# Kernel optimization log

Hardware: AMD Instinct MI355X
Metric: run time of the kernel (lower is better)

The kernel has to match this reference:

```python
import jax, jax.numpy as jnp
import numpy as np

H = 128            # hidden_dim
R = 16             # num_rbf
L = 3              # num_atom_encoder_layers
LAT = 32           # latent_dim
NUM_ATOM_TYPES = 64
CUTOFF = 5.0       # atom_cutoff
N_RES = 2048
DEG = 16           # avg radius-graph degree
_PATTERN = np.array([19, 20, 21, 22, 23, 24, 25, 22])  # ragged atoms/residue, mean 22


def setup_inputs() -> dict:
    key = jax.random.key(0)
    ks = jax.random.split(key, 16)
    apr = np.tile(_PATTERN, N_RES // len(_PATTERN))        # (N,) atoms per residue
    A = int(apr.sum())                                     # 45056 atoms
    E = A * DEG                                            # 720896 edges
    rng = np.random.default_rng(0)

    def gl(k, shape, fan_in):
        return jax.random.normal(k, shape, jnp.float32) * (fan_in ** -0.5)

    return {
        "atom_coords": jax.random.normal(ks[0], (A, 3), jnp.float32) * 10.0,
        "atom_types": jax.random.randint(ks[1], (A,), 0, NUM_ATOM_TYPES),
        "residue_indices": jnp.asarray(np.repeat(np.arange(N_RES), apr)),
        "residue_types": jax.random.randint(ks[2], (N_RES,), 0, 4),
        "atoms_per_residue": jnp.asarray(apr),
        "edge_src": jnp.asarray(rng.integers(0, A, E)),
        "edge_dst": jnp.asarray(rng.integers(0, A, E)),
        # learned parameters
        "atom_embed": gl(ks[3], (NUM_ATOM_TYPES, H), 1.0),
        "residue_embed": gl(ks[4], (4, H), 1.0),
        "We1": gl(ks[5], (L, 2 * H + R, H), 2 * H + R), "be1": jnp.zeros((L, H)),
        "We2": gl(ks[6], (L, H, H), H), "be2": jnp.zeros((L, H)),
        "Wh1": gl(ks[7], (L, 2 * H, H), 2 * H), "bh1": jnp.zeros((L, H)),
        "Wh2": gl(ks[8], (L, H, H), H), "bh2": jnp.zeros((L, H)),
        "Wq": gl(ks[9], (H, H), H), "bq": jnp.zeros((H,)),
        "Wk": gl(ks[10], (H, H), H), "bk": jnp.zeros((H,)),
        "Wv": gl(ks[11], (H, H), H), "bv": jnp.zeros((H,)),
        "Wmu": gl(ks[12], (H, LAT), H), "bmu": jnp.zeros((LAT,)),
        "Wlv": gl(ks[13], (H, LAT), H) * 0.01, "blv": jnp.full((LAT,), -2.0),
    }


def reference(atom_coords, atom_types, residue_indices, residue_types,
              atoms_per_residue, edge_src, edge_dst,
              atom_embed, residue_embed,
              We1, be1, We2, be2, Wh1, bh1, Wh2, bh2,
              Wq, bq, Wk, bk, Wv, bv, Wmu, bmu, Wlv, blv):
    A = atom_coords.shape[0]
    N = residue_types.shape[0]
    coords = atom_coords - atom_coords.mean(0, keepdims=True)  # center_coords

    # Gaussian radial basis expansion of edge distances
    d = jnp.linalg.norm(coords[edge_src] - coords[edge_dst], axis=-1)  # (E,)
    centers = jnp.linspace(0.0, CUTOFF, R)
    gamma = (R / CUTOFF) ** 2
    edge_attr = jnp.exp(-gamma * (d[:, None] - centers) ** 2)          # (E,R)

    # atom features: atom-type embed + residue-type embed scattered to atoms
    res_emb = residue_embed[residue_types]                             # (N,H)
    h = atom_embed[atom_types] + res_emb[residue_indices]              # (A,H)

    # EGNN layers (update_coords=False): message MLP -> sum-agg -> residual node MLP
    for l in range(L):
        m = jnp.concatenate([h[edge_src], h[edge_dst], edge_attr], axis=-1)  # (E,2H+R)
        m = jax.nn.silu(m @ We1[l] + be1[l])
        m = jax.nn.silu(m @ We2[l] + be2[l])                                  # (E,H)
        agg = jax.ops.segment_sum(m, edge_dst, num_segments=A)               # (A,H)
        u = jnp.concatenate([h, agg], axis=-1)                               # (A,2H)
        u = jax.nn.silu(u @ Wh1[l] + bh1[l])
        h = h + (u @ Wh2[l] + bh2[l])

    # segment (per-residue) attention pooling of atoms -> residues
    q = res_emb @ Wq + bq                                              # (N,H)
    k = h @ Wk + bk                                                    # (A,H)
    v = h @ Wv + bv                                                    # (A,H)
    scores = jnp.sum(q[residue_indices] * k, axis=-1) * (H ** -0.5)    # (A,)
    smax = jax.ops.segment_max(scores, residue_indices, num_segments=N)
    ex = jnp.exp(scores - smax[residue_indices])
    denom = jax.ops.segment_sum(ex, residue_indices, num_segments=N)
    w = ex / denom[residue_indices]
    pooled = jax.ops.segment_sum(w[:, None] * v, residue_indices, num_segments=N)  # (N,H)

    mu = pooled @ Wmu + bmu
    logvar = jnp.clip(pooled @ Wlv + blv, -10.0, 2.0)
    return mu, logvar
```

## Files before the change

### kernel.cpp

```cpp
#include <hip/hip_runtime.h>
#include <hip/hip_bf16.h>

#define H 128
#define LATD 32

typedef __attribute__((ext_vector_type(8))) _Float16 half8t;
typedef __attribute__((ext_vector_type(4))) _Float16 half4t;
typedef __attribute__((ext_vector_type(8))) unsigned short u16x8;
typedef __attribute__((ext_vector_type(4))) float f32x4;

#define OFF_RBF 0
#define OFF_W2  12288
#define OFF_PROJ 61440
#define OFF_H1  159744
#define OFF_H2  258048
#define WP_TOTAL 307200

__device__ __forceinline__ float silu_f(float x) {
  return x * __builtin_amdgcn_rcpf(1.0f + __expf(-x));
}
__device__ __forceinline__ unsigned short f16u(float x) {
  _Float16 hh = (_Float16)x;
  return *(unsigned short*)&hh;
}

template<int K>
__device__ __forceinline__ void mm4x4(const float* X0, int ldx,
                                      const float* __restrict__ W, int c0,
                                      float acc[4][4]) {
  #pragma unroll 4
  for (int k = 0; k < K; k += 4) {
    float4 xv[4], w4[4];
    #pragma unroll
    for (int rr = 0; rr < 4; ++rr) xv[rr] = *(const float4*)(X0 + rr * ldx + k);
    #pragma unroll
    for (int kk = 0; kk < 4; ++kk) w4[kk] = *(const float4*)(W + (size_t)(k + kk) * H + c0);
    const float* x = (const float*)xv;
    const float* w = (const float*)w4;
    #pragma unroll
    for (int rr = 0; rr < 4; ++rr)
      #pragma unroll
      for (int cc = 0; cc < 4; ++cc)
        acc[rr][cc] += x[rr*4+0]*w[cc] + x[rr*4+1]*w[4+cc] +
                       x[rr*4+2]*w[8+cc] + x[rr*4+3]*w[12+cc];
  }
}

__global__ void k_init_h(const float* __restrict__ atom_embed,
                         const float* __restrict__ residue_embed,
                         const int* __restrict__ atype,
                         const int* __restrict__ ridx,
                         const int* __restrict__ rtype,
                         float* __restrict__ h, unsigned short* __restrict__ hb, int A) {
  int i = blockIdx.x * blockDim.x + threadIdx.x;
  if (i >= A * H) return;
  int a = i >> 7, j = i & 127;
  float v = atom_embed[atype[a] * H + j] + residue_embed[rtype[ridx[a]] * H + j];
  h[i] = v;
  hb[i] = f16u(v);
}

__global__ void k_dist(const float* __restrict__ coords,
                       const int* __restrict__ esrc, const int* __restrict__ edst,
                       float* __restrict__ dbuf, int E) {
  int e = blockIdx.x * blockDim.x + threadIdx.x;
  if (e >= E) return;
  int s = esrc[e], t = edst[e];
  float dx = coords[3*s+0] - coords[3*t+0];
  float dy = coords[3*s+1] - coords[3*t+1];
  float dz = coords[3*s+2] - coords[3*t+2];
  dbuf[e] = sqrtf(dx*dx + dy*dy + dz*dz);
}

__global__ void k_starts(const int* __restrict__ ridx, int* __restrict__ starts, int A) {
  int a = blockIdx.x * blockDim.x + threadIdx.x;
  if (a >= A) return;
  if (a == 0 || ridx[a] != ridx[a-1]) starts[ridx[a]] = a;
}

__global__ void k_hist(const int* __restrict__ edst, int* __restrict__ cnt, int E) {
  int e = blockIdx.x * blockDim.x + threadIdx.x;
  if (e < E) atomicAdd(&cnt[edst[e]], 1);
}

__global__ __launch_bounds__(1024) void k_scanA(const int* __restrict__ cnt,
                                                int* __restrict__ cursor,
                                                int* __restrict__ bsum, int A) {
  __shared__ int buf[1024];
  int tid = threadIdx.x;
  int i = blockIdx.x * 1024 + tid;
  int v = (i < A) ? cnt[i] : 0;
  buf[tid] = v;
  __syncthreads();
  #pragma unroll
  for (int off = 1; off < 1024; off <<= 1) {
    int nv = (tid >= off) ? buf[tid - off] : 0;
    __syncthreads();
    buf[tid] += nv;
    __syncthreads();
  }
  if (i < A) cursor[i] = buf[tid] - v;
  if (tid == 1023) bsum[blockIdx.x] = buf[1023];
}

__global__ void k_scanB(int* __restrict__ bsum, int nb) {
  int lane = threadIdx.x;
  int v = (lane < nb) ? bsum[lane] : 0;
  int s = v;
  #pragma unroll
  for (int off = 1; off < 64; off <<= 1) {
    int nv = __shfl_up(s, off);
    if (lane >= off) s += nv;
  }
  if (lane < nb) bsum[lane] = s - v;
}

__global__ void k_scanC(int* __restrict__ cursor, const int* __restrict__ bsum, int A) {
  int i = blockIdx.x * blockDim.x + threadIdx.x;
  if (i < A) cursor[i] += bsum[i >> 10];
}

__global__ void k_scatter(const int* __restrict__ edst, int* __restrict__ cursor,
                          int* __restrict__ eperm, int E) {
  int e = blockIdx.x * blockDim.x + threadIdx.x;
  if (e >= E) return;
  int p = atomicAdd(&cursor[edst[e]], 1);
  eperm[p] = e;
}

__global__ void k_pack(const float* __restrict__ We1, const float* __restrict__ We2,
                       const float* __restrict__ Wh1, const float* __restrict__ Wh2,
                       unsigned short* __restrict__ wp) {
  int t = blockIdx.x * blockDim.x + threadIdx.x;
  if (t >= WP_TOTAL) return;
  if (t < OFF_W2) {
    int u = t - OFF_RBF; int layer = u / 4096, idx = u % 4096;
    int i = idx & 7, lane = (idx >> 3) & 63, ct = (idx >> 9) & 7;
    int k = ((lane >> 4) * 8) + i;
    int c = ct * 16 + (lane & 15);
    const float* src = We1 + (size_t)layer * 272 * H;
    wp[t] = f16u(k < 16 ? src[(size_t)(256 + k) * H + c] : 0.0f);
  } else if (t < OFF_PROJ) {
    int u = t - OFF_W2; int layer = u / 16384, idx = u % 16384;
    int i = idx & 7, lane = (idx >> 3) & 63, ct = (idx >> 9) & 7, kt = idx >> 12;
    int k = kt * 32 + (lane >> 4) * 8 + i, c = ct * 16 + (lane & 15);
    const float* src = We2 + (size_t)layer * 128 * H;
    wp[t] = f16u(src[(size_t)k * H + c]);
  } else if (t < OFF_H1) {
    int u = t - OFF_PROJ; int layer = u / 32768, idx = u % 32768;
    int i = idx & 7, lane = (idx >> 3) & 63, ct = (idx >> 9) & 15, kt = idx >> 13;
    int k = kt * 32 + (lane >> 4) * 8 + i, c = ct * 16 + (lane & 15);
    const float* src = We1 + (size_t)layer * 272 * H;
    float v = (c < 128) ? src[(size_t)k * H + c] : src[(size_t)(128 + k) * H + (c - 128)];
    wp[t] = f16u(v);
  } else if (t < OFF_H2) {
    int u = t - OFF_H1; int layer = u / 32768, idx = u % 32768;
    int i = idx & 7, lane = (idx >> 3) & 63, ct = (idx >> 9) & 7, kt = idx >> 12;
    int k = kt * 32 + (lane >> 4) * 8 + i, c = ct * 16 + (lane & 15);
    const float* src = Wh1 + (size_t)layer * 256 * H;
    wp[t] = f16u(src[(size_t)k * H + c]);
  } else {
    int u = t - OFF_H2; int layer = u / 16384, idx = u % 16384;
    int i = idx & 7, lane = (idx >> 3) & 63, ct = (idx >> 9) & 7, kt = idx >> 12;
    int k = kt * 32 + (lane >> 4) * 8 + i, c = ct * 16 + (lane & 15);
    const float* src = Wh2 + (size_t)layer * 128 * H;
    wp[t] = f16u(src[(size_t)k * H + c]);
  }
}

__global__ __launch_bounds__(256) void k_proj(
    const unsigned short* __restrict__ hb, const unsigned short* __restrict__ Wp,
    unsigned short* __restrict__ Ph, int A) {
  const int tid = threadIdx.x, l = tid & 63, wv = tid >> 6;
  const int lr = l & 15, lk = (l >> 4) * 8;
  const int a0 = blockIdx.x * 64;
  f32x4 acc[4][4] = {};
  #pragma unroll
  for (int kt = 0; kt < 4; ++kt) {
    half8t a[4], b[4];
    #pragma unroll
    for (int rt = 0; rt < 4; ++rt) {
      int row = a0 + rt * 16 + lr; if (row >= A) row = A - 1;
      a[rt] = *(const half8t*)&hb[(size_t)row * H + kt * 32 + lk];
    }
    #pragma unroll
    for (int ci = 0; ci < 4; ++ci)
      b[ci] = *(const half8t*)&Wp[(((size_t)kt * 16 + wv * 4 + ci) * 64 + l) * 8];
    #pragma unroll
    for (int rt = 0; rt < 4; ++rt)
      #pragma unroll
      for (int ci = 0; ci < 4; ++ci)
        acc[rt][ci] = __builtin_amdgcn_mfma_f32_16x16x32_f16(a[rt], b[ci], acc[rt][ci], 0, 0, 0);
  }
  #pragma unroll
  for (int rt = 0; rt < 4; ++rt)
    #pragma unroll
    for (int ci = 0; ci < 4; ++ci) {
      int col = (wv * 4 + ci) * 16 + lr;
      #pragma unroll
      for (int rr = 0; rr < 4; ++rr) {
        int row = a0 + rt * 16 + (l >> 4) * 4 + rr;
        if (row < A) Ph[(size_t)row * 256 + col] = f16u(acc[rt][ci][rr]);
      }
    }
}

#define PS 136
#define RS 40
#define M1S 136
#define M2SF 132

__global__ __launch_bounds__(256) void k_edge_mfma(
    const unsigned short* __restrict__ Ph, const float* __restrict__ dbuf,
    const int* __restrict__ esrc, const int* __restrict__ edst,
    const int* __restrict__ eperm,
    const unsigned short* __restrict__ Wr, const float* __restrict__ be1,
    const unsigned short* __restrict__ W2p, const float* __restrict__ be2,
    float* __restrict__ agg, int E) {
  __shared__ __align__(16) unsigned short SH[64*PS + 64*RS + 64*M1S];
  __shared__ int dstv[64];
  unsigned short* Psum = SH;
  unsigned short* rbfs = SH + 64 * PS;
  unsigned short* M1s  = SH + 64 * (PS + RS);
  float* M2s = (float*)SH;

  const int tid = threadIdx.x;
  const int e0 = blockIdx.x * 64;
  {
    const int r = tid >> 2, qt = tid & 3;
    int e = e0 + r;
    int ec = (e < E) ? e : (E - 1);
    int es = eperm[ec];
    int s = esrc[es], t = edst[es];
    if (qt == 0) dstv[r] = (e < E) ? t : -1;
    const half8t* ps = (const half8t*)(Ph + (size_t)s * 256);
    const half8t* pt = (const half8t*)(Ph + (size_t)t * 256 + 128);
    half8t* pr = (half8t*)&Psum[r * PS];
    #pragma unroll
    for (int i = 0; i < 4; ++i)
      pr[qt * 4 + i] = ps[qt * 4 + i] + pt[qt * 4 + i];
    if (qt < 2) {
      float d = dbuf[es];
      #pragma unroll
      for (int i = 0; i < 8; ++i) {
        int j = qt * 8 + i;
        float dd = d - (float)j * (5.0f / 15.0f);
        rbfs[r * RS + j] = f16u(__expf(-10.24f * dd * dd));
      }
    } else if (qt == 2) {
      #pragma unroll
      for (int i = 0; i < 16; ++i) rbfs[r * RS + 16 + i] = 0;
    }
  }
  __syncthreads();

  const int l = tid & 63, wv = tid >> 6;
  const int lr = l & 15, lk = (l >> 4) * 8, g4 = (l >> 4) * 4;
  const int ct0 = wv * 2;

  f32x4 acc[2][4];
  #pragma unroll
  for (int cj = 0; cj < 2; ++cj) {
    int cbase = (ct0 + cj) * 16 + g4;
    #pragma unroll
    for (int et = 0; et < 4; ++et) {
      half4t p4 = *(const half4t*)&Psum[(et * 16 + lr) * PS + cbase];
      acc[cj][et][0] = (float)p4[0];
      acc[cj][et][1] = (float)p4[1];
      acc[cj][et][2] = (float)p4[2];
      acc[cj][et][3] = (float)p4[3];
    }
  }
  {
    half8t ar[2];
    #pragma unroll
    for (int cj = 0; cj < 2; ++cj)
      ar[cj] = *(const half8t*)&Wr[(((size_t)(ct0 + cj)) * 64 + l) * 8];
    #pragma unroll
    for (int et = 0; et < 4; ++et) {
      half8t br = *(const half8t*)&rbfs[(et * 16 + lr) * RS + lk];
      #pragma unroll
      for (int cj = 0; cj < 2; ++cj)
        acc[cj][et] = __builtin_amdgcn_mfma_f32_16x16x32_f16(ar[cj], br, acc[cj][et], 0, 0, 0);
    }
  }
  #pragma unroll
  for (int cj = 0; cj < 2; ++cj) {
    f32x4 b1v = *(const f32x4*)&be1[(ct0 + cj) * 16 + g4];
    #pragma unroll
    for (int et = 0; et < 4; ++et) {
      half4t m4;
      #pragma unroll
      for (int rr = 0; rr < 4; ++rr)
        m4[rr] = (_Float16)silu_f(acc[cj][et][rr] + b1v[rr]);
      *(half4t*)&M1s[(et * 16 + lr) * M1S + (ct0 + cj) * 16 + g4] = m4;
    }
  }
  __syncthreads();

  f32x4 acc2[2][4] = {};
  #pragma unroll
  for (int kt = 0; kt < 4; ++kt) {
    half8t a2[2], b2[4];
    #pragma unroll
    for (int cj = 0; cj < 2; ++cj)
      a2[cj] = *(const half8t*)&W2p[(((size_t)kt * 8 + ct0 + cj) * 64 + l) * 8];
    #pragma unroll
    for (int et = 0; et < 4; ++et)
      b2[et] = *(const half8t*)&M1s[(et * 16 + lr) * M1S + kt * 32 + lk];
    #pragma unroll
    for (int cj = 0; cj < 2; ++cj)
      #pragma unroll
      for (int et = 0; et < 4; ++et)
        acc2[cj][et] = __builtin_amdgcn_mfma_f32_16x16x32_f16(a2[cj], b2[et], acc2[cj][et], 0, 0, 0);
  }
  __syncthreads();
  #pragma unroll
  for (int cj = 0; cj < 2; ++cj) {
    f32x4 b2v = *(const f32x4*)&be2[(ct0 + cj) * 16 + g4];
    #pragma unroll
    for (int et = 0; et < 4; ++et) {
      f32x4 w;
      #pragma unroll
      for (int rr = 0; rr < 4; ++rr)
        w[rr] = silu_f(acc2[cj][et][rr] + b2v[rr]);
      *(f32x4*)&M2s[(et * 16 + lr) * M2SF + (ct0 + cj) * 16 + g4] = w;
    }
  }
  __syncthreads();

  {
    int cp = tid & 63, qr = tid >> 6;
    int rbeg = qr * 16, rend = rbeg + 16;
    float a0 = 0.f, a1 = 0.f;
    int prev = -1;
    for (int r = rbeg; r < rend; ++r) {
      int dv = dstv[r];
      float2 v = *(const float2*)&M2s[r * M2SF + cp * 2];
      if (dv != prev) {
        if (prev >= 0) {
          atomicAdd(&agg[(size_t)prev * H + cp * 2], a0);
          atomicAdd(&agg[(size_t)prev * H + cp * 2 + 1], a1);
        }
        a0 = a1 = 0.f;
        prev = dv;
      }
      if (dv >= 0) { a0 += v.x; a1 += v.y; }
    }
    if (prev >= 0) {
      atomicAdd(&agg[(size_t)prev * H + cp * 2], a0);
      atomicAdd(&agg[(size_t)prev * H + cp * 2 + 1], a1);
    }
  }
}

#define NXS 264

__global__ __launch_bounds__(256) void k_node_mfma(
    float* __restrict__ h, unsigned short* __restrict__ hb,
    const float* __restrict__ agg,
    const unsigned short* __restrict__ W1p, const float* __restrict__ bh1,
    const unsigned short* __restrict__ W2p, const float* __restrict__ bh2, int A) {
  __shared__ __align__(16) unsigned short Xs[32 * NXS];
  __shared__ __align__(16) unsigned short Us[32 * M1S];
  const int tid = threadIdx.x;
  const int a0 = blockIdx.x * 32;
  {
    const int r = tid >> 3, oct = tid & 7;
    int a = a0 + r; if (a >= A) a = A - 1;
    const u16x8* hr = (const u16x8*)(hb + (size_t)a * H);
    u16x8* xr = (u16x8*)&Xs[r * NXS];
    xr[oct * 2]     = hr[oct * 2];
    xr[oct * 2 + 1] = hr[oct * 2 + 1];
    const float4* ar = (const float4*)(agg + (size_t)a * H);
    u16x8 tmp[2];
    unsigned short* tp = (unsigned short*)tmp;
    #pragma unroll
    for (int i = 0; i < 4; ++i) {
      float4 av = ar[oct * 4 + i];
      tp[i*4+0] = f16u(av.x); tp[i*4+1] = f16u(av.y);
      tp[i*4+2] = f16u(av.z); tp[i*4+3] = f16u(av.w);
    }
    xr[16 + oct * 2]     = tmp[0];
    xr[16 + oct * 2 + 1] = tmp[1];
  }
  __syncthreads();

  const int l = tid & 63, wv = tid >> 6;
  const int lr = l & 15, lk = (l >> 4) * 8;
  const int ct0 = wv * 2;
  const int c0 = ct0 * 16 + lr, c1 = c0 + 16;
  const float b1a = bh1[c0], b1b = bh1[c1];
  const float b2a = bh2[c0], b2b = bh2[c1];

  f32x4 acc[2][2] = {};
  #pragma unroll
  for (int kt = 0; kt < 8; ++kt) {
    half8t a[2], b[2];
    #pragma unroll
    for (int rt = 0; rt < 2; ++rt)
      a[rt] = *(const half8t*)&Xs[(rt * 16 + lr) * NXS + kt * 32 + lk];
    #pragma unroll
    for (int j = 0; j < 2; ++j)
      b[j] = *(const half8t*)&W1p[(((size_t)kt * 8 + ct0 + j) * 64 + l) * 8];
    #pragma unroll
    for (int rt = 0; rt < 2; ++rt)
      #pragma unroll
      for (int j = 0; j < 2; ++j)
        acc[rt][j] = __builtin_amdgcn_mfma_f32_16x16x32_f16(a[rt], b[j], acc[rt][j], 0, 0, 0);
  }
  #pragma unroll
  for (int rt = 0; rt < 2; ++rt)
    #pragma unroll
    for (int j = 0; j < 2; ++j) {
      float bb = j ? b1b : b1a;
      int col = (ct0 + j) * 16 + lr;
      #pragma unroll
      for (int rr = 0; rr < 4; ++rr) {
        int row = rt * 16 + (l >> 4) * 4 + rr;
        Us[row * M1S + col] = f16u(silu_f(acc[rt][j][rr] + bb));
      }
    }
  __syncthreads();

  f32x4 acc2[2][2] = {};
  #pragma unroll
  for (int kt = 0; kt < 4; ++kt) {
    half8t a[2], b[2];
    #pragma unroll
    for (int rt = 0; rt < 2; ++rt)
      a[rt] = *(const half8t*)&Us[(rt * 16 + lr) * M1S + kt * 32 + lk];
    #pragma unroll
    for (int j = 0; j < 2; ++j)
      b[j] = *(const half8t*)&W2p[(((size_t)kt * 8 + ct0 + j) * 64 + l) * 8];
    #pragma unroll
    for (int rt = 0; rt < 2; ++rt)
      #pragma unroll
      for (int j = 0; j < 2; ++j)
        acc2[rt][j] = __builtin_amdgcn_mfma_f32_16x16x32_f16(a[rt], b[j], acc2[rt][j], 0, 0, 0);
  }
  #pragma unroll
  for (int rt = 0; rt < 2; ++rt)
    #pragma unroll
    for (int j = 0; j < 2; ++j) {
      float bb = j ? b2b : b2a;
      int col = (ct0 + j) * 16 + lr;
      #pragma unroll
      for (int rr = 0; rr < 4; ++rr) {
        int row = rt * 16 + (l >> 4) * 4 + rr;
        int a = a0 + row;
        if (a < A) {
          size_t off = (size_t)a * H + col;
          float nh = h[off] + acc2[rt][j][rr] + bb;
          h[off] = nh;
          hb[off] = f16u(nh);
        }
      }
    }
}

__global__ __launch_bounds__(256) void k_linear2(
    const float* __restrict__ in,
    const float* __restrict__ W1, const float* __restrict__ b1, float* __restrict__ out1,
    const float* __restrict__ W2, const float* __restrict__ b2, float* __restrict__ out2,
    int nrows) {
  __shared__ float X[32][132];
  const int tid = threadIdx.x, lane = tid & 63, wv = tid >> 6;
  const int r0 = blockIdx.x * 32;
  #pragma unroll
  for (int i = 0; i < 8; ++i) {
    int r = wv * 8 + i;
    int a = r0 + r; if (a >= nrows) a = nrows - 1;
    X[r][lane]      = in[(size_t)a*H + lane];
    X[r][64 + lane] = in[(size_t)a*H + 64 + lane];
  }
  __syncthreads();
  const int rowg = tid >> 5, c0 = (tid & 31) * 4;
  {
    float acc[4][4] = {};
    mm4x4<128>(&X[rowg*4][0], 132, W1, c0, acc);
    #pragma unroll
    for (int rr = 0; rr < 4; ++rr) {
      int a = r0 + rowg*4 + rr;
      if (a < nrows)
        #pragma unroll
        for (int cc = 0; cc < 4; ++cc)
          out1[(size_t)a*H + c0 + cc] = acc[rr][cc] + b1[c0+cc];
    }
  }
  {
    float acc[4][4] = {};
    mm4x4<128>(&X[rowg*4][0], 132, W2, c0, acc);
    #pragma unroll
    for (int rr = 0; rr < 4; ++rr) {
      int a = r0 + rowg*4 + rr;
      if (a < nrows)
        #pragma unroll
        for (int cc = 0; cc < 4; ++cc)
          out2[(size_t)a*H + c0 + cc] = acc[rr][cc] + b2[c0+cc];
    }
  }
}

__global__ void k_q(const float* __restrict__ residue_embed,
                    const int* __restrict__ rtype,
                    const float* __restrict__ Wq, const float* __restrict__ bq,
                    float* __restrict__ q, int N) {
  int i = blockIdx.x * blockDim.x + threadIdx.x;
  if (i >= N * H) return;
  int r = i >> 7, j = i & 127;
  const float* emb = residue_embed + (size_t)rtype[r] * H;
  float s = bq[j];
  #pragma unroll 4
  for (int k = 0; k < H; ++k) s += emb[k] * Wq[(size_t)k*H + j];
  q[i] = s;
}

__global__ __launch_bounds__(256) void k_pool(
    const float* __restrict__ q, const float* __restrict__ kbuf,
    const float* __restrict__ vbuf, const int* __restrict__ starts,
    const int* __restrict__ apr, float* __restrict__ pooled, int N) {
  int r = blockIdx.x * 4 + (threadIdx.x >> 6);
  if (r >= N) return;
  int lane = threadIdx.x & 63;
  int s0 = starts[r], cnt = apr[r];
  float q0 = q[(size_t)r*H + lane], q1 = q[(size_t)r*H + 64 + lane];
  float myscore = -1e30f;
  for (int i = 0; i < cnt; ++i) {
    size_t a = (size_t)(s0 + i) * H;
    float p = q0 * kbuf[a + lane] + q1 * kbuf[a + 64 + lane];
    #pragma unroll
    for (int off = 32; off; off >>= 1) p += __shfl_xor(p, off);
    if (lane == i) myscore = p * 0.08838834764831845f;
  }
  float val = (lane < cnt) ? myscore : -1e30f;
  float mx = val;
  #pragma unroll
  for (int off = 32; off; off >>= 1) mx = fmaxf(mx, __shfl_xor(mx, off));
  float ex = (lane < cnt) ? __expf(val - mx) : 0.0f;
  float sum = ex;
  #pragma unroll
  for (int off = 32; off; off >>= 1) sum += __shfl_xor(sum, off);
  float w = ex * __builtin_amdgcn_rcpf(sum);
  float p0 = 0.f, p1 = 0.f;
  for (int i = 0; i < cnt; ++i) {
    float wi = __shfl(w, i);
    size_t a = (size_t)(s0 + i) * H;
    p0 += wi * vbuf[a + lane];
    p1 += wi * vbuf[a + 64 + lane];
  }
  pooled[(size_t)r*H + lane] = p0;
  pooled[(size_t)r*H + 64 + lane] = p1;
}

__global__ void k_head(const float* __restrict__ pooled,
                       const float* __restrict__ Wmu, const float* __restrict__ bmu,
                       const float* __restrict__ Wlv, const float* __restrict__ blv,
                       float* __restrict__ out, int N) {
  int i = blockIdx.x * blockDim.x + threadIdx.x;
  if (i >= N * LATD) return;
  int r = i >> 5, j = i & 31;
  const float* p = pooled + (size_t)r * H;
  float smu = 0.f, slv = 0.f;
  #pragma unroll 4
  for (int k = 0; k < H; ++k) {
    float pv = p[k];
    smu += pv * Wmu[(size_t)k*LATD + j];
    slv += pv * Wlv[(size_t)k*LATD + j];
  }
  smu += bmu[j];
  slv += blv[j];
  slv = fminf(fmaxf(slv, -10.0f), 2.0f);
  out[i] = smu;
  out[(size_t)N*LATD + i] = slv;
}

extern "C" void kernel_launch(void* const* d_in, const int* in_sizes, int n_in,
                              void* d_out, int out_size, void* d_ws, size_t ws_size,
                              hipStream_t stream) {
  const float* coords        = (const float*)d_in[0];
  const int*   atype         = (const int*)d_in[1];
  const int*   ridx          = (const int*)d_in[2];
  const int*   rtype         = (const int*)d_in[3];
  const int*   apr           = (const int*)d_in[4];
  const int*   esrc          = (const int*)d_in[5];
  const int*   edst          = (const int*)d_in[6];
  const float* atom_embed    = (const float*)d_in[7];
  const float* residue_embed = (const float*)d_in[8];
  const float* We1 = (const float*)d_in[9];
  const float* be1 = (const float*)d_in[10];
  const float* We2 = (const float*)d_in[11];
  const float* be2 = (const float*)d_in[12];
  const float* Wh1 = (const float*)d_in[13];
  const float* bh1 = (const float*)d_in[14];
  const float* Wh2 = (const float*)d_in[15];
  const float* bh2 = (const float*)d_in[16];
  const float* Wq  = (const float*)d_in[17];
  const float* bq  = (const float*)d_in[18];
  const float* Wk  = (const float*)d_in[19];
  const float* bk  = (const float*)d_in[20];
  const float* Wv  = (const float*)d_in[21];
  const float* bv  = (const float*)d_in[22];
  const float* Wmu = (const float*)d_in[23];
  const float* bmu = (const float*)d_in[24];
  const float* Wlv = (const float*)d_in[25];
  const float* blv = (const float*)d_in[26];

  const int A = in_sizes[1];
  const int N = in_sizes[3];
  const int E = in_sizes[5];

  float* ws     = (float*)d_ws;
  float* h      = ws;
  float* agg    = h + (size_t)A * H;
  float* vbuf   = agg + (size_t)A * H;
  float* dbuf   = vbuf + (size_t)A * H;
  float* qbuf   = dbuf + (size_t)E;
  float* pooled = qbuf + (size_t)N * H;
  int*   starts = (int*)(pooled + (size_t)N * H);
  unsigned short* hbuf = (unsigned short*)(starts + N);
  int*   eperm  = (int*)(hbuf + (size_t)A * H);
  int*   cnt    = eperm + (size_t)E;
  int*   cursor = cnt + A;
  int*   bsum   = cursor + A;
  unsigned short* wp = (unsigned short*)(bsum + 64);
  unsigned short* Ph = (unsigned short*)vbuf;

  k_init_h<<<(A * H + 255) / 256, 256, 0, stream>>>(atom_embed, residue_embed,
                                                    atype, ridx, rtype, h, hbuf, A);
  k_dist<<<(E + 255) / 256, 256, 0, stream>>>(coords, esrc, edst, dbuf, E);
  k_starts<<<(A + 255) / 256, 256, 0, stream>>>(ridx, starts, A);
  k_pack<<<(WP_TOTAL + 255) / 256, 256, 0, stream>>>(We1, We2, Wh1, Wh2, wp);

  const int nb = (A + 1023) / 1024;
  hipMemsetAsync(cnt, 0, (size_t)A * sizeof(int), stream);
  k_hist<<<(E + 255) / 256, 256, 0, stream>>>(edst, cnt, E);
  k_scanA<<<nb, 1024, 0, stream>>>(cnt, cursor, bsum, A);
  k_scanB<<<1, 64, 0, stream>>>(bsum, nb);
  k_scanC<<<(A + 255) / 256, 256, 0, stream>>>(cursor, bsum, A);
  k_scatter<<<(E + 255) / 256, 256, 0, stream>>>(edst, cursor, eperm, E);

  for (int l = 0; l < 3; ++l) {
    hipMemsetAsync(agg, 0, (size_t)A * H * sizeof(float), stream);
    k_proj<<<(A + 63) / 64, 256, 0, stream>>>(
        hbuf, wp + OFF_PROJ + (size_t)l * 32768, Ph, A);
    k_edge_mfma<<<(E + 63) / 64, 256, 0, stream>>>(
        Ph, dbuf, esrc, edst, eperm,
        wp + OFF_RBF + (size_t)l * 4096,  be1 + (size_t)l * H,
        wp + OFF_W2  + (size_t)l * 16384, be2 + (size_t)l * H, agg, E);
    k_node_mfma<<<(A + 31) / 32, 256, 0, stream>>>(
        h, hbuf, agg,
        wp + OFF_H1 + (size_t)l * 32768, bh1 + (size_t)l * H,
        wp + OFF_H2 + (size_t)l * 16384, bh2 + (size_t)l * H, A);
  }

  k_q<<<(N * H + 255) / 256, 256, 0, stream>>>(residue_embed, rtype, Wq, bq, qbuf, N);
  float* kbuf = agg;
  k_linear2<<<(A + 31) / 32, 256, 0, stream>>>(h, Wk, bk, kbuf, Wv, bv, vbuf, A);
  k_pool<<<(N + 3) / 4, 256, 0, stream>>>(qbuf, kbuf, vbuf, starts, apr, pooled, N);
  k_head<<<(N * LATD + 255) / 256, 256, 0, stream>>>(pooled, Wmu, bmu, Wlv, blv,
                                                     (float*)d_out, N);
}
```

Measured before the change: 664.4 us.

## Gather edge inputs directly in registers, fp16 M2 staging, MFMA K/V projection

The edge kernel no longer stages the summed projections and RBF values in shared memory. Each lane gathers the source and target projection rows from global memory into registers and computes the RBF fragments in place, and the second-stage message tile is staged in fp16 instead of fp32. The final K/V linear layers move from an fp32 scalar kernel to the existing MFMA projection kernel with packed fp16 weights and a bias. The query is computed once for each of the four residue types and indexed by type. This cuts shared memory use and traffic and speeds up the pooling prologue, at the cost of uncoalesced global gathers and fp16 rounding of K/V and of the messages before aggregation.

```diff
diff --git a/kernel.cpp b/kernel.cpp
--- a/kernel.cpp
+++ b/kernel.cpp
@@ -6,6 +6,7 @@
 
 typedef __attribute__((ext_vector_type(8))) _Float16 half8t;
 typedef __attribute__((ext_vector_type(4))) _Float16 half4t;
+typedef __attribute__((ext_vector_type(2))) _Float16 half2t;
 typedef __attribute__((ext_vector_type(8))) unsigned short u16x8;
 typedef __attribute__((ext_vector_type(4))) float f32x4;
 
@@ -14,7 +15,8 @@
 #define OFF_PROJ 61440
 #define OFF_H1  159744
 #define OFF_H2  258048
-#define WP_TOTAL 307200
+#define OFF_KV  307200
+#define WP_TOTAL 339968
 
 __device__ __forceinline__ float silu_f(float x) {
   return x * __builtin_amdgcn_rcpf(1.0f + __expf(-x));
@@ -22,28 +24,6 @@
 __device__ __forceinline__ unsigned short f16u(float x) {
   _Float16 hh = (_Float16)x;
   return *(unsigned short*)&hh;
-}
-
-template<int K>
-__device__ __forceinline__ void mm4x4(const float* X0, int ldx,
-                                      const float* __restrict__ W, int c0,
-                                      float acc[4][4]) {
-  #pragma unroll 4
-  for (int k = 0; k < K; k += 4) {
-    float4 xv[4], w4[4];
-    #pragma unroll
-    for (int rr = 0; rr < 4; ++rr) xv[rr] = *(const float4*)(X0 + rr * ldx + k);
-    #pragma unroll
-    for (int kk = 0; kk < 4; ++kk) w4[kk] = *(const float4*)(W + (size_t)(k + kk) * H + c0);
-    const float* x = (const float*)xv;
-    const float* w = (const float*)w4;
-    #pragma unroll
-    for (int rr = 0; rr < 4; ++rr)
-      #pragma unroll
-      for (int cc = 0; cc < 4; ++cc)
-        acc[rr][cc] += x[rr*4+0]*w[cc] + x[rr*4+1]*w[4+cc] +
-                       x[rr*4+2]*w[8+cc] + x[rr*4+3]*w[12+cc];
-  }
 }
 
 __global__ void k_init_h(const float* __restrict__ atom_embed,
@@ -78,6 +58,12 @@
   if (a == 0 || ridx[a] != ridx[a-1]) starts[ridx[a]] = a;
 }
 
+__global__ void k_bias2(const float* __restrict__ b1, const float* __restrict__ b2,
+                        float* __restrict__ bkv) {
+  int t = threadIdx.x;
+  bkv[t] = (t < 128) ? b1[t] : b2[t - 128];
+}
+
 __global__ void k_hist(const int* __restrict__ edst, int* __restrict__ cnt, int E) {
   int e = blockIdx.x * blockDim.x + threadIdx.x;
   if (e < E) atomicAdd(&cnt[edst[e]], 1);
@@ -130,6 +116,7 @@
 
 __global__ void k_pack(const float* __restrict__ We1, const float* __restrict__ We2,
                        const float* __restrict__ Wh1, const float* __restrict__ Wh2,
+                       const float* __restrict__ Wk,  const float* __restrict__ Wv,
                        unsigned short* __restrict__ wp) {
   int t = blockIdx.x * blockDim.x + threadIdx.x;
   if (t >= WP_TOTAL) return;
@@ -159,18 +146,24 @@
     int k = kt * 32 + (lane >> 4) * 8 + i, c = ct * 16 + (lane & 15);
     const float* src = Wh1 + (size_t)layer * 256 * H;
     wp[t] = f16u(src[(size_t)k * H + c]);
-  } else {
+  } else if (t < OFF_KV) {
     int u = t - OFF_H2; int layer = u / 16384, idx = u % 16384;
     int i = idx & 7, lane = (idx >> 3) & 63, ct = (idx >> 9) & 7, kt = idx >> 12;
     int k = kt * 32 + (lane >> 4) * 8 + i, c = ct * 16 + (lane & 15);
     const float* src = Wh2 + (size_t)layer * 128 * H;
     wp[t] = f16u(src[(size_t)k * H + c]);
+  } else {
+    int idx = t - OFF_KV;
+    int i = idx & 7, lane = (idx >> 3) & 63, ct = (idx >> 9) & 15, kt = idx >> 13;
+    int k = kt * 32 + (lane >> 4) * 8 + i, c = ct * 16 + (lane & 15);
+    float v = (c < 128) ? Wk[(size_t)k * H + c] : Wv[(size_t)k * H + (c - 128)];
+    wp[t] = f16u(v);
   }
 }
 
 __global__ __launch_bounds__(256) void k_proj(
     const unsigned short* __restrict__ hb, const unsigned short* __restrict__ Wp,
-    unsigned short* __restrict__ Ph, int A) {
+    unsigned short* __restrict__ Ph, int A, const float* __restrict__ bias) {
   const int tid = threadIdx.x, l = tid & 63, wv = tid >> 6;
   const int lr = l & 15, lk = (l >> 4) * 8;
   const int a0 = blockIdx.x * 64;
@@ -197,18 +190,17 @@
     #pragma unroll
     for (int ci = 0; ci < 4; ++ci) {
       int col = (wv * 4 + ci) * 16 + lr;
+      float bb = bias ? bias[col] : 0.0f;
       #pragma unroll
       for (int rr = 0; rr < 4; ++rr) {
         int row = a0 + rt * 16 + (l >> 4) * 4 + rr;
-        if (row < A) Ph[(size_t)row * 256 + col] = f16u(acc[rt][ci][rr]);
+        if (row < A) Ph[(size_t)row * 256 + col] = f16u(acc[rt][ci][rr] + bb);
       }
     }
 }
 
-#define PS 136
-#define RS 40
 #define M1S 136
-#define M2SF 132
+#define M2SH 132
 
 __global__ __launch_bounds__(256) void k_edge_mfma(
     const unsigned short* __restrict__ Ph, const float* __restrict__ dbuf,
@@ -217,72 +209,75 @@
     const unsigned short* __restrict__ Wr, const float* __restrict__ be1,
     const unsigned short* __restrict__ W2p, const float* __restrict__ be2,
     float* __restrict__ agg, int E) {
-  __shared__ __align__(16) unsigned short SH[64*PS + 64*RS + 64*M1S];
+  __shared__ __align__(16) unsigned short M1s[64 * M1S];
   __shared__ int dstv[64];
-  unsigned short* Psum = SH;
-  unsigned short* rbfs = SH + 64 * PS;
-  unsigned short* M1s  = SH + 64 * (PS + RS);
-  float* M2s = (float*)SH;
+  unsigned short* M2h = M1s;
 
   const int tid = threadIdx.x;
   const int e0 = blockIdx.x * 64;
-  {
-    const int r = tid >> 2, qt = tid & 3;
-    int e = e0 + r;
-    int ec = (e < E) ? e : (E - 1);
-    int es = eperm[ec];
-    int s = esrc[es], t = edst[es];
-    if (qt == 0) dstv[r] = (e < E) ? t : -1;
-    const half8t* ps = (const half8t*)(Ph + (size_t)s * 256);
-    const half8t* pt = (const half8t*)(Ph + (size_t)t * 256 + 128);
-    half8t* pr = (half8t*)&Psum[r * PS];
-    #pragma unroll
-    for (int i = 0; i < 4; ++i)
-      pr[qt * 4 + i] = ps[qt * 4 + i] + pt[qt * 4 + i];
-    if (qt < 2) {
-      float d = dbuf[es];
-      #pragma unroll
-      for (int i = 0; i < 8; ++i) {
-        int j = qt * 8 + i;
-        float dd = d - (float)j * (5.0f / 15.0f);
-        rbfs[r * RS + j] = f16u(__expf(-10.24f * dd * dd));
-      }
-    } else if (qt == 2) {
-      #pragma unroll
-      for (int i = 0; i < 16; ++i) rbfs[r * RS + 16 + i] = 0;
-    }
-  }
-  __syncthreads();
-
   const int l = tid & 63, wv = tid >> 6;
   const int lr = l & 15, lk = (l >> 4) * 8, g4 = (l >> 4) * 4;
   const int ct0 = wv * 2;
 
+  int sA[4], tA[4];
+  float dA[4];
+  #pragma unroll
+  for (int et = 0; et < 4; ++et) {
+    int e = e0 + et * 16 + lr;
+    int ec = (e < E) ? e : (E - 1);
+    int es = eperm[ec];
+    sA[et] = esrc[es];
+    tA[et] = edst[es];
+    dA[et] = dbuf[es];
+  }
+  if (tid < 64) {
+    int e = e0 + tid;
+    int ec = (e < E) ? e : (E - 1);
+    dstv[tid] = (e < E) ? edst[eperm[ec]] : -1;
+  }
+
   f32x4 acc[2][4];
   #pragma unroll
   for (int cj = 0; cj < 2; ++cj) {
     int cbase = (ct0 + cj) * 16 + g4;
     #pragma unroll
     for (int et = 0; et < 4; ++et) {
-      half4t p4 = *(const half4t*)&Psum[(et * 16 + lr) * PS + cbase];
-      acc[cj][et][0] = (float)p4[0];
-      acc[cj][et][1] = (float)p4[1];
-      acc[cj][et][2] = (float)p4[2];
-      acc[cj][et][3] = (float)p4[3];
+      half4t a = *(const half4t*)&Ph[(size_t)sA[et] * 256 + cbase];
+      half4t b = *(const half4t*)&Ph[(size_t)tA[et] * 256 + 128 + cbase];
+      half4t p = a + b;
+      acc[cj][et][0] = (float)p[0];
+      acc[cj][et][1] = (float)p[1];
+      acc[cj][et][2] = (float)p[2];
+      acc[cj][et][3] = (float)p[3];
     }
   }
   {
+    half8t br[4];
+    if (lk < 16) {
+      #pragma unroll
+      for (int et = 0; et < 4; ++et) {
+        float d = dA[et];
+        #pragma unroll
+        for (int i = 0; i < 8; ++i) {
+          float dd = d - (float)(lk + i) * (5.0f / 15.0f);
+          br[et][i] = (_Float16)__expf(-10.24f * dd * dd);
+        }
+      }
+    } else {
+      #pragma unroll
+      for (int et = 0; et < 4; ++et)
+        #pragma unroll
+        for (int i = 0; i < 8; ++i) br[et][i] = (_Float16)0.0f;
+    }
     half8t ar[2];
     #pragma unroll
     for (int cj = 0; cj < 2; ++cj)
       ar[cj] = *(const half8t*)&Wr[(((size_t)(ct0 + cj)) * 64 + l) * 8];
     #pragma unroll
-    for (int et = 0; et < 4; ++et) {
-      half8t br = *(const half8t*)&rbfs[(et * 16 + lr) * RS + lk];
+    for (int et = 0; et < 4; ++et)
       #pragma unroll
       for (int cj = 0; cj < 2; ++cj)
-        acc[cj][et] = __builtin_amdgcn_mfma_f32_16x16x32_f16(ar[cj], br, acc[cj][et], 0, 0, 0);
-    }
+        acc[cj][et] = __builtin_amdgcn_mfma_f32_16x16x32_f16(ar[cj], br[et], acc[cj][et], 0, 0, 0);
   }
   #pragma unroll
   for (int cj = 0; cj < 2; ++cj) {
@@ -320,11 +315,11 @@
     f32x4 b2v = *(const f32x4*)&be2[(ct0 + cj) * 16 + g4];
     #pragma unroll
     for (int et = 0; et < 4; ++et) {
-      f32x4 w;
+      half4t m4;
       #pragma unroll
       for (int rr = 0; rr < 4; ++rr)
-        w[rr] = silu_f(acc2[cj][et][rr] + b2v[rr]);
-      *(f32x4*)&M2s[(et * 16 + lr) * M2SF + (ct0 + cj) * 16 + g4] = w;
+        m4[rr] = (_Float16)silu_f(acc2[cj][et][rr] + b2v[rr]);
+      *(half4t*)&M2h[(et * 16 + lr) * M2SH + (ct0 + cj) * 16 + g4] = m4;
     }
   }
   __syncthreads();
@@ -336,7 +331,7 @@
     int prev = -1;
     for (int r = rbeg; r < rend; ++r) {
       int dv = dstv[r];
-      float2 v = *(const float2*)&M2s[r * M2SF + cp * 2];
+      half2t v = *(const half2t*)&M2h[r * M2SH + cp * 2];
       if (dv != prev) {
         if (prev >= 0) {
           atomicAdd(&agg[(size_t)prev * H + cp * 2], a0);
@@ -345,7 +340,7 @@
         a0 = a1 = 0.f;
         prev = dv;
       }
-      if (dv >= 0) { a0 += v.x; a1 += v.y; }
+      if (dv >= 0) { a0 += (float)v[0]; a1 += (float)v[1]; }
     }
     if (prev >= 0) {
       atomicAdd(&agg[(size_t)prev * H + cp * 2], a0);
@@ -459,76 +454,34 @@
     }
 }
 
-__global__ __launch_bounds__(256) void k_linear2(
-    const float* __restrict__ in,
-    const float* __restrict__ W1, const float* __restrict__ b1, float* __restrict__ out1,
-    const float* __restrict__ W2, const float* __restrict__ b2, float* __restrict__ out2,
-    int nrows) {
-  __shared__ float X[32][132];
-  const int tid = threadIdx.x, lane = tid & 63, wv = tid >> 6;
-  const int r0 = blockIdx.x * 32;
-  #pragma unroll
-  for (int i = 0; i < 8; ++i) {
-    int r = wv * 8 + i;
-    int a = r0 + r; if (a >= nrows) a = nrows - 1;
-    X[r][lane]      = in[(size_t)a*H + lane];
-    X[r][64 + lane] = in[(size_t)a*H + 64 + lane];
-  }
-  __syncthreads();
-  const int rowg = tid >> 5, c0 = (tid & 31) * 4;
-  {
-    float acc[4][4] = {};
-    mm4x4<128>(&X[rowg*4][0], 132, W1, c0, acc);
-    #pragma unroll
-    for (int rr = 0; rr < 4; ++rr) {
-      int a = r0 + rowg*4 + rr;
-      if (a < nrows)
-        #pragma unroll
-        for (int cc = 0; cc < 4; ++cc)
-          out1[(size_t)a*H + c0 + cc] = acc[rr][cc] + b1[c0+cc];
-    }
-  }
-  {
-    float acc[4][4] = {};
-    mm4x4<128>(&X[rowg*4][0], 132, W2, c0, acc);
-    #pragma unroll
-    for (int rr = 0; rr < 4; ++rr) {
-      int a = r0 + rowg*4 + rr;
-      if (a < nrows)
-        #pragma unroll
-        for (int cc = 0; cc < 4; ++cc)
-          out2[(size_t)a*H + c0 + cc] = acc[rr][cc] + b2[c0+cc];
-    }
-  }
-}
-
-__global__ void k_q(const float* __restrict__ residue_embed,
-                    const int* __restrict__ rtype,
-                    const float* __restrict__ Wq, const float* __restrict__ bq,
-                    float* __restrict__ q, int N) {
+__global__ void k_q4(const float* __restrict__ residue_embed,
+                     const float* __restrict__ Wq, const float* __restrict__ bq,
+                     float* __restrict__ q4) {
   int i = blockIdx.x * blockDim.x + threadIdx.x;
-  if (i >= N * H) return;
+  if (i >= 4 * H) return;
   int r = i >> 7, j = i & 127;
-  const float* emb = residue_embed + (size_t)rtype[r] * H;
+  const float* emb = residue_embed + (size_t)r * H;
   float s = bq[j];
   #pragma unroll 4
   for (int k = 0; k < H; ++k) s += emb[k] * Wq[(size_t)k*H + j];
-  q[i] = s;
+  q4[i] = s;
 }
 
 __global__ __launch_bounds__(256) void k_pool(
-    const float* __restrict__ q, const float* __restrict__ kbuf,
-    const float* __restrict__ vbuf, const int* __restrict__ starts,
+    const float* __restrict__ q4, const int* __restrict__ rtype,
+    const unsigned short* __restrict__ kv, const int* __restrict__ starts,
     const int* __restrict__ apr, float* __restrict__ pooled, int N) {
   int r = blockIdx.x * 4 + (threadIdx.x >> 6);
   if (r >= N) return;
   int lane = threadIdx.x & 63;
   int s0 = starts[r], cnt = apr[r];
-  float q0 = q[(size_t)r*H + lane], q1 = q[(size_t)r*H + 64 + lane];
+  const float* qrow = q4 + (size_t)rtype[r] * H;
+  float q0 = qrow[lane], q1 = qrow[64 + lane];
   float myscore = -1e30f;
   for (int i = 0; i < cnt; ++i) {
-    size_t a = (size_t)(s0 + i) * H;
-    float p = q0 * kbuf[a + lane] + q1 * kbuf[a + 64 + lane];
+    const unsigned short* kr = kv + (size_t)(s0 + i) * 256;
+    float p = q0 * (float)(*(const _Float16*)&kr[lane]) +
+              q1 * (float)(*(const _Float16*)&kr[64 + lane]);
     #pragma unroll
     for (int off = 32; off; off >>= 1) p += __shfl_xor(p, off);
     if (lane == i) myscore = p * 0.08838834764831845f;
@@ -545,9 +498,9 @@
   float p0 = 0.f, p1 = 0.f;
   for (int i = 0; i < cnt; ++i) {
     float wi = __shfl(w, i);
-    size_t a = (size_t)(s0 + i) * H;
-    p0 += wi * vbuf[a + lane];
-    p1 += wi * vbuf[a + 64 + lane];
+    const unsigned short* vr = kv + (size_t)(s0 + i) * 256 + 128;
+    p0 += wi * (float)(*(const _Float16*)&vr[lane]);
+    p1 += wi * (float)(*(const _Float16*)&vr[64 + lane]);
   }
   pooled[(size_t)r*H + lane] = p0;
   pooled[(size_t)r*H + 64 + lane] = p1;
@@ -615,8 +568,9 @@
   float* agg    = h + (size_t)A * H;
   float* vbuf   = agg + (size_t)A * H;
   float* dbuf   = vbuf + (size_t)A * H;
-  float* qbuf   = dbuf + (size_t)E;
-  float* pooled = qbuf + (size_t)N * H;
+  float* q4     = dbuf + (size_t)E;
+  float* bkv    = q4 + 4 * H;
+  float* pooled = bkv + 256;
   int*   starts = (int*)(pooled + (size_t)N * H);
   unsigned short* hbuf = (unsigned short*)(starts + N);
   int*   eperm  = (int*)(hbuf + (size_t)A * H);
@@ -630,7 +584,8 @@
                                                     atype, ridx, rtype, h, hbuf, A);
   k_dist<<<(E + 255) / 256, 256, 0, stream>>>(coords, esrc, edst, dbuf, E);
   k_starts<<<(A + 255) / 256, 256, 0, stream>>>(ridx, starts, A);
-  k_pack<<<(WP_TOTAL + 255) / 256, 256, 0, stream>>>(We1, We2, Wh1, Wh2, wp);
+  k_pack<<<(WP_TOTAL + 255) / 256, 256, 0, stream>>>(We1, We2, Wh1, Wh2, Wk, Wv, wp);
+  k_bias2<<<1, 256, 0, stream>>>(bk, bv, bkv);
 
   const int nb = (A + 1023) / 1024;
   hipMemsetAsync(cnt, 0, (size_t)A * sizeof(int), stream);
@@ -643,7 +598,7 @@
   for (int l = 0; l < 3; ++l) {
     hipMemsetAsync(agg, 0, (size_t)A * H * sizeof(float), stream);
     k_proj<<<(A + 63) / 64, 256, 0, stream>>>(
-        hbuf, wp + OFF_PROJ + (size_t)l * 32768, Ph, A);
+        hbuf, wp + OFF_PROJ + (size_t)l * 32768, Ph, A, nullptr);
     k_edge_mfma<<<(E + 63) / 64, 256, 0, stream>>>(
         Ph, dbuf, esrc, edst, eperm,
         wp + OFF_RBF + (size_t)l * 4096,  be1 + (size_t)l * H,
@@ -654,10 +609,10 @@
         wp + OFF_H2 + (size_t)l * 16384, bh2 + (size_t)l * H, A);
   }
 
-  k_q<<<(N * H + 255) / 256, 256, 0, stream>>>(residue_embed, rtype, Wq, bq, qbuf, N);
-  float* kbuf = agg;
-  k_linear2<<<(A + 31) / 32, 256, 0, stream>>>(h, Wk, bk, kbuf, Wv, bv, vbuf, A);
-  k_pool<<<(N + 3) / 4, 256, 0, stream>>>(qbuf, kbuf, vbuf, starts, apr, pooled, N);
+  k_q4<<<2, 256, 0, stream>>>(residue_embed, Wq, bq, q4);
+  unsigned short* kv = Ph;
+  k_proj<<<(A + 63) / 64, 256, 0, stream>>>(hbuf, wp + OFF_KV, kv, A, bkv);
+  k_pool<<<(N + 3) / 4, 256, 0, stream>>>(q4, rtype, kv, starts, apr, pooled, N);
   k_head<<<(N * LATD + 255) / 256, 256, 0, stream>>>(pooled, Wmu, bmu, Wlv, blv,
                                                      (float*)d_out, N);
 }
```

Result: slower. 720.4 us (+8.4%).
